# Kernel optimization log

Measured on AMD Instinct MI355X. Metric: run time of the kernel, lower is better.

## Reference

```python
import jax, jax.numpy as jnp
import numpy as np


def _rgcn(x, src, dst, et, basis, comp, root, bias):
    # Basis-decomposed RGCNConv (PyG semantics): per-relation mean aggregation
    # over incoming edges + root transform + bias.
    N = x.shape[0]
    R = comp.shape[0]
    W = jnp.einsum('rb,bio->rio', comp, basis)          # [R, in, out]
    xr = jnp.einsum('ni,rio->rno', x, W)                 # [R, N, out]
    msg = xr[et, src]                                    # [E, out] gather per edge
    seg = dst * R + et                                   # (target, relation) segment id
    cnt = jax.ops.segment_sum(jnp.ones(et.shape, x.dtype), seg, num_segments=N * R)
    norm = 1.0 / jnp.maximum(cnt, 1.0)                   # mean per (dst, relation)
    msg = msg * norm[seg][:, None]
    agg = jax.ops.segment_sum(msg, dst, num_segments=N)  # scatter-add to targets
    return agg + x @ root + bias


def setup_inputs() -> dict:
    key = jax.random.key(0)
    ks = jax.random.split(key, 20)
    N, E, R, B, F, D, C, NB = 100000, 1600000, 5, 512, 4, 32, 5, 2
    s = 0.1
    inp = {
        'x': jax.random.normal(ks[0], (N, F), jnp.float32),
        'edge_index': jax.random.randint(ks[1], (2, E), 0, N, dtype=jnp.int32),
        'edge_type': jax.random.randint(ks[2], (E,), 0, R, dtype=jnp.int32),
        'start_nodes': jax.random.randint(ks[3], (B,), 0, N, dtype=jnp.int32),
        # layer 0: in=F, out=D
        'basis0': jax.random.normal(ks[4], (NB, F, D), jnp.float32) * s,
        'comp0': jax.random.normal(ks[5], (R, NB), jnp.float32) * s,
        'root0': jax.random.normal(ks[6], (F, D), jnp.float32) * s,
        'bias0': jax.random.normal(ks[7], (D,), jnp.float32) * s,
        # layers 1..3: in=out=D, stacked
        'basis': jax.random.normal(ks[8], (3, NB, D, D), jnp.float32) * s,
        'comp': jax.random.normal(ks[9], (3, R, NB), jnp.float32) * s,
        'root': jax.random.normal(ks[10], (3, D, D), jnp.float32) * s,
        'bias': jax.random.normal(ks[11], (3, D), jnp.float32) * s,
        # MLP head: sum(latent_dim)=128 -> 128 -> C
        'lin1_w': jax.random.normal(ks[12], (4 * D, 128), jnp.float32) * s,
        'lin1_b': jax.random.normal(ks[13], (128,), jnp.float32) * s,
        'lin2_w': jax.random.normal(ks[14], (128, C), jnp.float32) * s,
        'lin2_b': jax.random.normal(ks[15], (C,), jnp.float32) * s,
    }
    return inp


def reference(x, edge_index, edge_type, start_nodes, basis0, comp0, root0, bias0,
              basis, comp, root, bias, lin1_w, lin1_b, lin2_w, lin2_b):
    src, dst = edge_index[0], edge_index[1]
    h = jnp.tanh(_rgcn(x, src, dst, edge_type, basis0, comp0, root0, bias0))
    states = [h]
    for l in range(basis.shape[0]):
        h = jnp.tanh(_rgcn(h, src, dst, edge_type, basis[l], comp[l], root[l], bias[l]))
        states.append(h)
    concat = jnp.concatenate(states, axis=1)             # [N, 128]
    # Per-graph readout: the walk's degenerate n_walks=1 branch, i.e. the
    # start (user) node's concatenated state (sequential backtracking walk
    # replaced by its deterministic initialization path; eval mode, no dropout).
    acc = concat[start_nodes]                            # [B, 128]
    h1 = jax.nn.relu(acc @ lin1_w + lin1_b)
    logits = h1 @ lin2_w + lin2_b
    return jax.nn.log_softmax(logits, axis=-1)
```

## Files before the change

kernel.cpp:

```cpp
#include <hip/hip_runtime.h>
#include <cstdint>

#define N_NODES 100000
#define N_EDGES 1600000
#define R_REL   5
#define NBASIS  2
#define B_START 512
#define PART_SZ 12500
#define NBUCK   256
#define BUCK_SZ 391
#define EPB     6250
#define STAGE_CAP 7000

typedef __attribute__((ext_vector_type(8))) short short8;
typedef __attribute__((ext_vector_type(4))) float f32x4;
typedef _Float16 half8 __attribute__((ext_vector_type(8)));

__device__ __forceinline__ unsigned short f2bf(float f) {
    unsigned u = __float_as_uint(f);
    unsigned r = (u + 0x7FFF + ((u >> 16) & 1)) >> 16;
    return (unsigned short)r;
}
__device__ __forceinline__ float bf2f(unsigned short u) {
    return __uint_as_float(((unsigned)u) << 16);
}
__device__ __forceinline__ unsigned short f2h(float f) {
    _Float16 h = (_Float16)f;
    return __builtin_bit_cast(unsigned short, h);
}


__global__ __launch_bounds__(256) void k_cntb(
    const int* __restrict__ ei, int* __restrict__ bhist) {
    __shared__ int lh[NBUCK];
    int tid = threadIdx.x;
    lh[tid] = 0;
    __syncthreads();
    int base = blockIdx.x * EPB;
    for (int j = tid; j < EPB; j += 256) {
        int dst = ei[N_EDGES + base + j];
        atomicAdd(&lh[dst / BUCK_SZ], 1);
    }
    __syncthreads();
    bhist[blockIdx.x * NBUCK + tid] = lh[tid];
}

__global__ __launch_bounds__(256) void k_colscan(
    int* __restrict__ bhist, int* __restrict__ colsum) {
    __shared__ int s[256];
    int b = blockIdx.x, i = threadIdx.x;
    int v = bhist[i * NBUCK + b];
    s[i] = v;
    __syncthreads();
    for (int o = 1; o < 256; o <<= 1) {
        int t = (i >= o) ? s[i - o] : 0;
        __syncthreads();
        s[i] += t;
        __syncthreads();
    }
    bhist[i * NBUCK + b] = s[i] - v;
    if (i == 255) colsum[b] = s[255];
}

__global__ __launch_bounds__(256) void k_tiny(
    const int* __restrict__ colsum, int* __restrict__ bbase) {
    __shared__ int s[256];
    int i = threadIdx.x;
    int v = colsum[i];
    s[i] = v;
    __syncthreads();
    for (int o = 1; o < 256; o <<= 1) {
        int t = (i >= o) ? s[i - o] : 0;
        __syncthreads();
        s[i] += t;
        __syncthreads();
    }
    bbase[i] = s[i] - v;
    if (i == 255) bbase[NBUCK] = s[255];
}

__global__ __launch_bounds__(256) void k_scat(
    const int* __restrict__ ei, const int* __restrict__ et,
    const int* __restrict__ bhist, const int* __restrict__ bbase,
    int* __restrict__ arena) {
    __shared__ int lc[NBUCK];
    int tid = threadIdx.x;
    lc[tid] = bhist[blockIdx.x * NBUCK + tid] + bbase[tid];
    __syncthreads();
    int base = blockIdx.x * EPB;
    for (int j = tid; j < EPB; j += 256) {
        int e   = base + j;
        int src = ei[e];
        int dst = ei[N_EDGES + e];
        int t   = et[e];
        int bk  = dst / BUCK_SZ;
        int dl  = dst - bk * BUCK_SZ;
        int pos = atomicAdd(&lc[bk], 1);
        arena[pos] = src | (t << 17) | (dl << 20);
    }
}

__global__ __launch_bounds__(256) void k_build(
    const int* __restrict__ arena, const int* __restrict__ bbase,
    int* __restrict__ off, int* __restrict__ pk_m, float* __restrict__ nv5,
    unsigned* __restrict__ degpk) {
    __shared__ int deg5[BUCK_SZ * R_REL];
    __shared__ int loff[BUCK_SZ + 1];
    __shared__ int cur5[BUCK_SZ * R_REL];
    __shared__ int stg[STAGE_CAP];
    __shared__ int tsum[256];
    int b = blockIdx.x, tid = threadIdx.x;
    int base = bbase[b], end = bbase[b + 1];
    int count = end - base;
    for (int i = tid; i < BUCK_SZ * R_REL; i += 256) deg5[i] = 0;
    __syncthreads();
    for (int i = tid; i < count; i += 256) {
        int r  = arena[base + i];
        int dl = ((unsigned)r) >> 20;
        int t  = (r >> 17) & 7;
        atomicAdd(&deg5[dl * R_REL + t], 1);
    }
    __syncthreads();
    for (int dl = tid; dl < BUCK_SZ; dl += 256) {
        loff[dl] = deg5[dl * R_REL + 0] + deg5[dl * R_REL + 1] +
                   deg5[dl * R_REL + 2] + deg5[dl * R_REL + 3] +
                   deg5[dl * R_REL + 4];
    }
    __syncthreads();
    int d0 = 2 * tid, d1 = 2 * tid + 1;
    int va = (d0 < BUCK_SZ) ? loff[d0] : 0;
    int vb = (d1 < BUCK_SZ) ? loff[d1] : 0;
    tsum[tid] = va + vb;
    __syncthreads();
    for (int o = 1; o < 256; o <<= 1) {
        int v = (tid >= o) ? tsum[tid - o] : 0;
        __syncthreads();
        tsum[tid] += v;
        __syncthreads();
    }
    int pre = tsum[tid] - (va + vb);
    if (d0 < BUCK_SZ) loff[d0] = pre;
    if (d1 < BUCK_SZ) loff[d1] = pre + va;
    __syncthreads();
    for (int dl = tid; dl < BUCK_SZ; dl += 256) {
        int nn = b * BUCK_SZ + dl;
        int run = loff[dl];
        unsigned dp = 0;
#pragma unroll
        for (int t = 0; t < R_REL; t++) {
            cur5[dl * R_REL + t] = run;
            int c = deg5[dl * R_REL + t];
            run += c;
            int cc = c > 63 ? 63 : c;
            dp |= ((unsigned)cc) << (6 * t);
        }
        if (nn < N_NODES) {
            off[nn]   = base + loff[dl];
            degpk[nn] = dp;
#pragma unroll
            for (int t = 0; t < R_REL; t++) {
                int c = deg5[dl * R_REL + t];
                nv5[nn * R_REL + t] = 1.0f / (float)(c > 0 ? c : 1);
            }
        }
    }
    if (b == NBUCK - 1 && tid == 0) off[N_NODES] = N_EDGES;
    __syncthreads();
    for (int i = tid; i < count; i += 256) {
        int r  = arena[base + i];
        int dl = ((unsigned)r) >> 20;
        int t  = (r >> 17) & 7;
        int rk = atomicAdd(&cur5[dl * R_REL + t], 1);
        if (rk < STAGE_CAP) stg[rk] = r;
    }
    __syncthreads();
    for (int i = tid; i < count; i += 256) {
        int r = stg[i < STAGE_CAP ? i : STAGE_CAP - 1];
        pk_m[base + i] = r & 0x1FFFF;
    }
}


__global__ __launch_bounds__(256) void k_wprep(
    const float* __restrict__ basis, const float* __restrict__ comp,
    const float* __restrict__ root,  const float* __restrict__ basis0,
    const float* __restrict__ comp0, const float* __restrict__ root0,
    unsigned short* __restrict__ wfh, unsigned short* __restrict__ wfr,
    unsigned short* __restrict__ wf0) {
    __shared__ float lw[5120];
    int tid = threadIdx.x;
    int l = blockIdx.x;
    if (l < 3) {
        for (int idx = tid; idx < 5120; idx += 256) {
            int r = idx >> 10, rem = idx & 1023, i = rem >> 5, o = rem & 31;
            lw[idx] = comp[l * 10 + r * 2 + 0] * basis[l * 2048 + i * 32 + o]
                    + comp[l * 10 + r * 2 + 1] * basis[l * 2048 + 1024 + i * 32 + o];
        }
        __syncthreads();
        for (int idx = tid; idx < 5120; idx += 256) {
            int ot = idx / 2560, rem = idx % 2560;
            int s = rem >> 9, ln = (rem >> 3) & 63, j = idx & 7;
            int o = ot * 16 + (ln & 15), kk = (ln >> 4) * 8 + j;
            wfh[l * 5120 + idx] = f2h(lw[s * 1024 + kk * 32 + o]);
        }
        for (int idx = tid; idx < 2048; idx += 256) {
            int ot = idx >> 10, s = (idx >> 9) & 1, ln = (idx >> 3) & 63, j = idx & 7;
            int o = ot * 16 + (ln & 15), kk = (ln >> 4) * 8 + j;
            float val = root[l * 1024 + kk * 32 + o];
            unsigned short hi = f2bf(val);
            wfr[l * 2048 + idx] = s ? f2bf(val - bf2f(hi)) : hi;
        }
    } else {
        for (int idx = tid; idx < 1024; idx += 256) {
            int k = idx >> 5, o = idx & 31;
            float val = 0.f;
            if (k < 20) {
                int r = k >> 2, i = k & 3;
                val = comp0[r * 2 + 0] * basis0[i * 32 + o]
                    + comp0[r * 2 + 1] * basis0[128 + i * 32 + o];
            } else if (k < 24) val = root0[(k - 20) * 32 + o];
            lw[idx] = val;
        }
        __syncthreads();
        for (int idx = tid; idx < 1024; idx += 256) {
            int ot = idx >> 9, ln = (idx >> 3) & 63, j = idx & 7;
            int o = ot * 16 + (ln & 15), kk = (ln >> 4) * 8 + j;
            wf0[idx] = f2h(lw[kk * 32 + o]);
        }
    }
}


__global__ __launch_bounds__(256) void k_cvt0(
    const float* __restrict__ x, unsigned short* __restrict__ hb0) {
    int n = blockIdx.x * 256 + threadIdx.x;
    if (n >= N_NODES) return;
    float4 xv = *(const float4*)(x + (size_t)n * 4);
    unsigned short h0 = f2bf(xv.x), h1 = f2bf(xv.y), h2 = f2bf(xv.z), h3 = f2bf(xv.w);
    unsigned long long ph = (unsigned long long)h0 | ((unsigned long long)h1 << 16)
                          | ((unsigned long long)h2 << 32) | ((unsigned long long)h3 << 48);
    *(unsigned long long*)(hb0 + (size_t)n * 4) = ph;
}


__global__ __launch_bounds__(256) void k_gath32(
    const unsigned short* __restrict__ hb, const int* __restrict__ pk_m,
    const float* __restrict__ nv5, const unsigned* __restrict__ degpk,
    const int* __restrict__ off, unsigned short* __restrict__ agg) {
    int tid  = threadIdx.x;
    int lane32 = tid & 31;
    int sub  = tid >> 5;
    int part  = blockIdx.x & 7;
    int local = (blockIdx.x >> 3) * 8 + sub;
    if (local >= PART_SZ) return;
    int n = part * PART_SZ + local;
    int cpos = lane32 & 7;
    int slot = lane32 >> 3;
    const uint2* __restrict__ hb2 = (const uint2*)hb;

    int e0 = off[n];
    unsigned dp = degpk[n];
    int chunkbase = e0;
    int mreg = (chunkbase + lane32 < N_EDGES) ? pk_m[chunkbase + lane32] : 0;
    int e = e0;
#pragma unroll
    for (int r = 0; r < R_REL; r++) {
        int cnt = (int)((dp >> (6 * r)) & 63u);
        float nv = nv5[n * R_REL + r];
        float a0 = 0.f, a1 = 0.f, a2 = 0.f, a3 = 0.f;
        for (int kb = 0; kb < cnt; kb += 4) {
            if (e + kb + 3 >= chunkbase + 32) {
                chunkbase = e + kb;
                mreg = (chunkbase + lane32 < N_EDGES) ? pk_m[chunkbase + lane32] : 0;
            }
            int kq = kb + slot;
            int mq = __shfl(mreg, e + kq - chunkbase, 32);
            uint2 u = hb2[(size_t)mq * 8 + cpos];
            float msk = (kq < cnt) ? nv : 0.f;
            a0 += msk * __uint_as_float(u.x << 16);
            a1 += msk * __uint_as_float(u.x & 0xFFFF0000u);
            a2 += msk * __uint_as_float(u.y << 16);
            a3 += msk * __uint_as_float(u.y & 0xFFFF0000u);
        }
        e += cnt;
        a0 += __shfl_xor(a0, 8, 32);  a0 += __shfl_xor(a0, 16, 32);
        a1 += __shfl_xor(a1, 8, 32);  a1 += __shfl_xor(a1, 16, 32);
        a2 += __shfl_xor(a2, 8, 32);  a2 += __shfl_xor(a2, 16, 32);
        a3 += __shfl_xor(a3, 8, 32);  a3 += __shfl_xor(a3, 16, 32);
        if (slot == 0) {
            uint2 pk;
            pk.x = (unsigned)f2h(a0) | ((unsigned)f2h(a1) << 16);
            pk.y = (unsigned)f2h(a2) | ((unsigned)f2h(a3) << 16);
            *(uint2*)(agg + (size_t)n * 160 + r * 32 + cpos * 4) = pk;
        }
    }
}


__global__ __launch_bounds__(256) void k_gath0(
    const unsigned short* __restrict__ hb0, const float* __restrict__ x,
    const int* __restrict__ pk_m, const float* __restrict__ nv5,
    const unsigned* __restrict__ degpk, const int* __restrict__ off,
    unsigned short* __restrict__ a0v) {
    int tid  = threadIdx.x;
    int lane32 = tid & 31;
    int sub  = tid >> 5;
    int part  = blockIdx.x & 7;
    int local = (blockIdx.x >> 3) * 8 + sub;
    if (local >= PART_SZ) return;
    int n = part * PART_SZ + local;
    int cpos = lane32 & 1;
    int slot = lane32 >> 1;
    const unsigned* __restrict__ hb32 = (const unsigned*)hb0;

    int e0 = off[n];
    unsigned dp = degpk[n];
    int chunkbase = e0;
    int mreg = (chunkbase + lane32 < N_EDGES) ? pk_m[chunkbase + lane32] : 0;
    int e = e0;
#pragma unroll
    for (int r = 0; r < R_REL; r++) {
        int cnt = (int)((dp >> (6 * r)) & 63u);
        float nv = nv5[n * R_REL + r];
        float p0 = 0.f, p1 = 0.f;
        for (int kb = 0; kb < cnt; kb += 16) {
            if (e + kb + 15 >= chunkbase + 32) {
                chunkbase = e + kb;
                mreg = (chunkbase + lane32 < N_EDGES) ? pk_m[chunkbase + lane32] : 0;
            }
            int kq = kb + slot;
            int mq = __shfl(mreg, e + kq - chunkbase, 32);
            unsigned u = hb32[(size_t)mq * 2 + cpos];
            float msk = (kq < cnt) ? nv : 0.f;
            p0 += msk * __uint_as_float(u << 16);
            p1 += msk * __uint_as_float(u & 0xFFFF0000u);
        }
        e += cnt;
        p0 += __shfl_xor(p0, 2, 32); p0 += __shfl_xor(p0, 4, 32);
        p0 += __shfl_xor(p0, 8, 32); p0 += __shfl_xor(p0, 16, 32);
        p1 += __shfl_xor(p1, 2, 32); p1 += __shfl_xor(p1, 4, 32);
        p1 += __shfl_xor(p1, 8, 32); p1 += __shfl_xor(p1, 16, 32);
        if (slot == 0) {
            unsigned pk = (unsigned)f2h(p0) | ((unsigned)f2h(p1) << 16);
            *(unsigned*)(a0v + (size_t)n * 32 + r * 4 + cpos * 2) = pk;
        }
    }
    if (lane32 < 12) {
        float xv = (lane32 < 4) ? x[(size_t)n * 4 + lane32] : 0.f;
        a0v[(size_t)n * 32 + 20 + lane32] = (lane32 < 4) ? f2h(xv) : (unsigned short)0;
    }
}


__global__ __launch_bounds__(256) void k_gemm(
    const unsigned short* __restrict__ agg, const unsigned short* __restrict__ hbin,
    const unsigned short* __restrict__ wfhl, const unsigned short* __restrict__ wfrl,
    const float* __restrict__ biasL, float* __restrict__ h,
    unsigned short* __restrict__ hbout) {
    int tid = threadIdx.x;
    int wid = tid >> 6, lane = tid & 63;
    int tile = blockIdx.x * 4 + wid;
    if (tile >= N_NODES / 16) return;
    int n0 = tile * 16;
    int row = lane & 15, kg = lane >> 4;
    const half8* ar = (const half8*)(agg + (size_t)(n0 + row) * 160 + kg * 8);
    const half8* wh = (const half8*)wfhl;
    const short8* wr = (const short8*)wfrl;
    short8 hbf = *(const short8*)(hbin + (size_t)(n0 + row) * 32 + kg * 8);
    f32x4 c0 = {0.f, 0.f, 0.f, 0.f}, c1 = {0.f, 0.f, 0.f, 0.f};
#pragma unroll
    for (int s = 0; s < 5; s++) {
        half8 a = ar[s * 4];
        c0 = __builtin_amdgcn_mfma_f32_16x16x32_f16(a, wh[s * 64 + lane], c0, 0, 0, 0);
        c1 = __builtin_amdgcn_mfma_f32_16x16x32_f16(a, wh[320 + s * 64 + lane], c1, 0, 0, 0);
    }
    c0 = __builtin_amdgcn_mfma_f32_16x16x32_bf16(hbf, wr[lane], c0, 0, 0, 0);
    c0 = __builtin_amdgcn_mfma_f32_16x16x32_bf16(hbf, wr[64 + lane], c0, 0, 0, 0);
    c1 = __builtin_amdgcn_mfma_f32_16x16x32_bf16(hbf, wr[128 + lane], c1, 0, 0, 0);
    c1 = __builtin_amdgcn_mfma_f32_16x16x32_bf16(hbf, wr[192 + lane], c1, 0, 0, 0);
    float b0 = biasL[row], b1 = biasL[16 + row];
#pragma unroll
    for (int i = 0; i < 4; i++) {
        int n = n0 + kg * 4 + i;
        float t0 = tanhf(c0[i] + b0);
        float t1 = tanhf(c1[i] + b1);
        h[(size_t)n * 32 + row]      = t0;
        h[(size_t)n * 32 + 16 + row] = t1;
        hbout[(size_t)n * 32 + row]      = f2bf(t0);
        hbout[(size_t)n * 32 + 16 + row] = f2bf(t1);
    }
}

__global__ __launch_bounds__(256) void k_gemm0(
    const unsigned short* __restrict__ a0v, const unsigned short* __restrict__ wf0,
    const float* __restrict__ biasL, float* __restrict__ h,
    unsigned short* __restrict__ hbout) {
    int tid = threadIdx.x;
    int wid = tid >> 6, lane = tid & 63;
    int tile = blockIdx.x * 4 + wid;
    if (tile >= N_NODES / 16) return;
    int n0 = tile * 16;
    int row = lane & 15, kg = lane >> 4;
    half8 a = *(const half8*)(a0v + (size_t)(n0 + row) * 32 + kg * 8);
    const half8* wv = (const half8*)wf0;
    f32x4 c0 = {0.f, 0.f, 0.f, 0.f}, c1 = {0.f, 0.f, 0.f, 0.f};
    c0 = __builtin_amdgcn_mfma_f32_16x16x32_f16(a, wv[lane], c0, 0, 0, 0);
    c1 = __builtin_amdgcn_mfma_f32_16x16x32_f16(a, wv[64 + lane], c1, 0, 0, 0);
    float b0 = biasL[row], b1 = biasL[16 + row];
#pragma unroll
    for (int i = 0; i < 4; i++) {
        int n = n0 + kg * 4 + i;
        float t0 = tanhf(c0[i] + b0);
        float t1 = tanhf(c1[i] + b1);
        h[(size_t)n * 32 + row]      = t0;
        h[(size_t)n * 32 + 16 + row] = t1;
        hbout[(size_t)n * 32 + row]      = f2bf(t0);
        hbout[(size_t)n * 32 + 16 + row] = f2bf(t1);
    }
}


__global__ void k_save(const float* __restrict__ h, const int* __restrict__ start,
                       float* __restrict__ sav) {
    int t = blockIdx.x * blockDim.x + threadIdx.x;
    if (t < B_START * 32) {
        int b = t >> 5, ln = t & 31;
        sav[t] = h[(size_t)start[b] * 32 + ln];
    }
}

__global__ __launch_bounds__(128) void k_mlp(
    const float* __restrict__ sav, const float* __restrict__ w1,
    const float* __restrict__ b1, const float* __restrict__ w2,
    const float* __restrict__ b2, float* __restrict__ out) {
    __shared__ float cvec[128];
    __shared__ float hb[128];
    __shared__ float lg[8];
    int b = blockIdx.x, t = threadIdx.x;
    cvec[t] = sav[(t >> 5) * (B_START * 32) + b * 32 + (t & 31)];
    __syncthreads();
    float a = b1[t];
#pragma unroll 8
    for (int k = 0; k < 128; k++) a += cvec[k] * w1[k * 128 + t];
    hb[t] = fmaxf(a, 0.f);
    __syncthreads();
    if (t < 5) {
        float a2 = b2[t];
        for (int k = 0; k < 128; k++) a2 += hb[k] * w2[k * 5 + t];
        lg[t] = a2;
    }
    __syncthreads();
    if (t < 5) {
        float m = lg[0];
        for (int j = 1; j < 5; j++) m = fmaxf(m, lg[j]);
        float s = 0.f;
        for (int j = 0; j < 5; j++) s += expf(lg[j] - m);
        out[b * 5 + t] = lg[t] - m - logf(s);
    }
}


extern "C" void kernel_launch(void* const* d_in, const int* in_sizes, int n_in,
                              void* d_out, int out_size, void* d_ws, size_t ws_size,
                              hipStream_t stream) {
    const float* x      = (const float*)d_in[0];
    const int*   ei     = (const int*)d_in[1];
    const int*   etype  = (const int*)d_in[2];
    const int*   start  = (const int*)d_in[3];
    const float* basis0 = (const float*)d_in[4];
    const float* comp0  = (const float*)d_in[5];
    const float* root0  = (const float*)d_in[6];
    const float* bias0  = (const float*)d_in[7];
    const float* basis  = (const float*)d_in[8];
    const float* comp   = (const float*)d_in[9];
    const float* root   = (const float*)d_in[10];
    const float* bias   = (const float*)d_in[11];
    const float* w1     = (const float*)d_in[12];
    const float* b1     = (const float*)d_in[13];
    const float* w2     = (const float*)d_in[14];
    const float* b2     = (const float*)d_in[15];
    float* out = (float*)d_out;

    char* p = (char*)d_ws;
    auto alloc = [&](size_t bytes) -> void* {
        void* r = (void*)p;
        p += (bytes + 255) & ~(size_t)255;
        return r;
    };
    int*            bhist  = (int*)alloc((size_t)NBUCK * NBUCK * 4);
    int*            colsum = (int*)alloc(NBUCK * 4);
    int*            bbase  = (int*)alloc((NBUCK + 1) * 4);
    int*            arena  = (int*)alloc((size_t)N_EDGES * 4);
    int*            off    = (int*)alloc((N_NODES + 1) * 4);
    int*            pk_m   = (int*)alloc((size_t)N_EDGES * 4);
    float*          nv5    = (float*)alloc((size_t)N_NODES * R_REL * 4);
    unsigned*       degpk  = (unsigned*)alloc((size_t)N_NODES * 4);
    float*          h      = (float*)alloc((size_t)N_NODES * 32 * 4);
    unsigned short* hbuf   = (unsigned short*)alloc((size_t)(N_NODES + 64) * 32 * 2);
    unsigned short* hb0    = (unsigned short*)alloc((size_t)N_NODES * 4 * 2);
    unsigned short* a0v    = (unsigned short*)alloc((size_t)(N_NODES + 64) * 32 * 2);
    unsigned short* agg    = (unsigned short*)alloc((size_t)(N_NODES + 64) * 160 * 2);
    unsigned short* wfh    = (unsigned short*)alloc((size_t)3 * 5120 * 2);
    unsigned short* wfr    = (unsigned short*)alloc((size_t)3 * 2048 * 2);
    unsigned short* wf0    = (unsigned short*)alloc((size_t)1024 * 2);
    float*          sav    = (float*)alloc(4 * B_START * 32 * 4);

    k_cntb<<<NBUCK, 256, 0, stream>>>(ei, bhist);
    k_colscan<<<NBUCK, 256, 0, stream>>>(bhist, colsum);
    k_tiny<<<1, 256, 0, stream>>>(colsum, bbase);
    k_scat<<<NBUCK, 256, 0, stream>>>(ei, etype, bhist, bbase, arena);
    k_build<<<NBUCK, 256, 0, stream>>>(arena, bbase, off, pk_m, nv5, degpk);
    k_wprep<<<4, 256, 0, stream>>>(basis, comp, root, basis0, comp0, root0,
                                   wfh, wfr, wf0);
    k_cvt0<<<(N_NODES + 255) / 256, 256, 0, stream>>>(x, hb0);

    int nbGath = 8 * ((PART_SZ + 7) / 8);
    int nbGemm = (N_NODES / 16 + 3) / 4;

    k_gath0<<<nbGath, 256, 0, stream>>>(hb0, x, pk_m, nv5, degpk, off, a0v);
    k_gemm0<<<nbGemm, 256, 0, stream>>>(a0v, wf0, bias0, h, hbuf);
    k_save<<<64, 256, 0, stream>>>(h, start, sav);
    for (int l = 0; l < 3; l++) {
        k_gath32<<<nbGath, 256, 0, stream>>>(hbuf, pk_m, nv5, degpk, off, agg);
        k_gemm<<<nbGemm, 256, 0, stream>>>(agg, hbuf, wfh + (size_t)l * 5120,
                                           wfr + (size_t)l * 2048, bias + l * 32,
                                           h, hbuf);
        k_save<<<64, 256, 0, stream>>>(h, start, sav + (l + 1) * 16384);
    }

    k_mlp<<<B_START, 128, 0, stream>>>(sav, w1, b1, w2, b2, out);
}
```

Before: 380.1 us.

## Assign one lane group per relation in gather kernels with prefetched indices

The gather kernels are restructured so that each relation of a node gets its own group of lanes. Each group walks that relation's edges sequentially, prefetching the next edge index, and uses wider 16-byte or 8-byte feature loads. This replaces the old scheme of shuffle-broadcast edge chunks, masked slots and cross-slot shuffle reductions, which wasted lanes on low-degree relations. It also drops the partition-interleaved block mapping and adds nontemporal loads and stores for the streamed index and aggregate buffers. In exchange, per-lane serial loops follow per-relation degree, which may cause divergence and imbalance, and the three lanes with s >= 5 in each 8-lane group sit idle.

```diff
diff --git a/kernel.cpp b/kernel.cpp
--- a/kernel.cpp
+++ b/kernel.cpp
@@ -6,7 +6,6 @@
 #define R_REL   5
 #define NBASIS  2
 #define B_START 512
-#define PART_SZ 12500
 #define NBUCK   256
 #define BUCK_SZ 391
 #define EPB     6250
@@ -15,6 +14,8 @@
 typedef __attribute__((ext_vector_type(8))) short short8;
 typedef __attribute__((ext_vector_type(4))) float f32x4;
 typedef _Float16 half8 __attribute__((ext_vector_type(8)));
+typedef unsigned uint32x2 __attribute__((ext_vector_type(2)));
+typedef unsigned uint32x4 __attribute__((ext_vector_type(4)));
 
 __device__ __forceinline__ unsigned short f2bf(float f) {
     unsigned u = __float_as_uint(f);
@@ -247,52 +248,50 @@
     const unsigned short* __restrict__ hb, const int* __restrict__ pk_m,
     const float* __restrict__ nv5, const unsigned* __restrict__ degpk,
     const int* __restrict__ off, unsigned short* __restrict__ agg) {
-    int tid  = threadIdx.x;
+    int tid = threadIdx.x;
+    int n = blockIdx.x * 8 + (tid >> 5);
     int lane32 = tid & 31;
-    int sub  = tid >> 5;
-    int part  = blockIdx.x & 7;
-    int local = (blockIdx.x >> 3) * 8 + sub;
-    if (local >= PART_SZ) return;
-    int n = part * PART_SZ + local;
-    int cpos = lane32 & 7;
-    int slot = lane32 >> 3;
-    const uint2* __restrict__ hb2 = (const uint2*)hb;
+    int s = lane32 >> 2;
+    int cpos = lane32 & 3;
 
     int e0 = off[n];
     unsigned dp = degpk[n];
-    int chunkbase = e0;
-    int mreg = (chunkbase + lane32 < N_EDGES) ? pk_m[chunkbase + lane32] : 0;
-    int e = e0;
-#pragma unroll
-    for (int r = 0; r < R_REL; r++) {
-        int cnt = (int)((dp >> (6 * r)) & 63u);
-        float nv = nv5[n * R_REL + r];
-        float a0 = 0.f, a1 = 0.f, a2 = 0.f, a3 = 0.f;
-        for (int kb = 0; kb < cnt; kb += 4) {
-            if (e + kb + 3 >= chunkbase + 32) {
-                chunkbase = e + kb;
-                mreg = (chunkbase + lane32 < N_EDGES) ? pk_m[chunkbase + lane32] : 0;
-            }
-            int kq = kb + slot;
-            int mq = __shfl(mreg, e + kq - chunkbase, 32);
-            uint2 u = hb2[(size_t)mq * 8 + cpos];
-            float msk = (kq < cnt) ? nv : 0.f;
-            a0 += msk * __uint_as_float(u.x << 16);
-            a1 += msk * __uint_as_float(u.x & 0xFFFF0000u);
-            a2 += msk * __uint_as_float(u.y << 16);
-            a3 += msk * __uint_as_float(u.y & 0xFFFF0000u);
-        }
-        e += cnt;
-        a0 += __shfl_xor(a0, 8, 32);  a0 += __shfl_xor(a0, 16, 32);
-        a1 += __shfl_xor(a1, 8, 32);  a1 += __shfl_xor(a1, 16, 32);
-        a2 += __shfl_xor(a2, 8, 32);  a2 += __shfl_xor(a2, 16, 32);
-        a3 += __shfl_xor(a3, 8, 32);  a3 += __shfl_xor(a3, 16, 32);
-        if (slot == 0) {
-            uint2 pk;
-            pk.x = (unsigned)f2h(a0) | ((unsigned)f2h(a1) << 16);
-            pk.y = (unsigned)f2h(a2) | ((unsigned)f2h(a3) << 16);
-            *(uint2*)(agg + (size_t)n * 160 + r * 32 + cpos * 4) = pk;
-        }
+    int c0 = dp & 63, c1 = (dp >> 6) & 63, c2 = (dp >> 12) & 63,
+        c3 = (dp >> 18) & 63, c4 = (dp >> 24) & 63;
+    int cnt = s == 0 ? c0 : s == 1 ? c1 : s == 2 ? c2 : s == 3 ? c3
+            : s == 4 ? c4 : 0;
+    int start = (s > 0 ? c0 : 0) + (s > 1 ? c1 : 0) + (s > 2 ? c2 : 0)
+              + (s > 3 ? c3 : 0);
+    float nv = (s < R_REL) ? nv5[n * R_REL + s] : 0.f;
+
+    const uint32x4* __restrict__ hb4 = (const uint32x4*)hb;
+    float a0 = 0.f, a1 = 0.f, a2 = 0.f, a3 = 0.f;
+    float a4 = 0.f, a5 = 0.f, a6 = 0.f, a7 = 0.f;
+    int base = e0 + start;
+    int pb = base < N_EDGES ? base : N_EDGES - 1;
+    int mcur = __builtin_nontemporal_load(pk_m + pb);
+    for (int k = 0; k < cnt; ++k) {
+        int kn = k + 1 < cnt ? k + 1 : cnt - 1;
+        int mnxt = __builtin_nontemporal_load(pk_m + base + kn);
+        uint32x4 u = hb4[(size_t)mcur * 4 + cpos];
+        a0 += nv * __uint_as_float(u.x << 16);
+        a1 += nv * __uint_as_float(u.x & 0xFFFF0000u);
+        a2 += nv * __uint_as_float(u.y << 16);
+        a3 += nv * __uint_as_float(u.y & 0xFFFF0000u);
+        a4 += nv * __uint_as_float(u.z << 16);
+        a5 += nv * __uint_as_float(u.z & 0xFFFF0000u);
+        a6 += nv * __uint_as_float(u.w << 16);
+        a7 += nv * __uint_as_float(u.w & 0xFFFF0000u);
+        mcur = mnxt;
+    }
+    if (s < R_REL) {
+        uint32x4 pk;
+        pk.x = (unsigned)f2h(a0) | ((unsigned)f2h(a1) << 16);
+        pk.y = (unsigned)f2h(a2) | ((unsigned)f2h(a3) << 16);
+        pk.z = (unsigned)f2h(a4) | ((unsigned)f2h(a5) << 16);
+        pk.w = (unsigned)f2h(a6) | ((unsigned)f2h(a7) << 16);
+        __builtin_nontemporal_store(pk,
+            (uint32x4*)(agg + (size_t)n * 160 + s * 32 + cpos * 8));
     }
 }
 
@@ -302,52 +301,53 @@
     const int* __restrict__ pk_m, const float* __restrict__ nv5,
     const unsigned* __restrict__ degpk, const int* __restrict__ off,
     unsigned short* __restrict__ a0v) {
-    int tid  = threadIdx.x;
-    int lane32 = tid & 31;
-    int sub  = tid >> 5;
-    int part  = blockIdx.x & 7;
-    int local = (blockIdx.x >> 3) * 8 + sub;
-    if (local >= PART_SZ) return;
-    int n = part * PART_SZ + local;
-    int cpos = lane32 & 1;
-    int slot = lane32 >> 1;
-    const unsigned* __restrict__ hb32 = (const unsigned*)hb0;
+    int tid = threadIdx.x;
+    int n = blockIdx.x * 32 + (tid >> 3);
+    int s = tid & 7;
 
     int e0 = off[n];
     unsigned dp = degpk[n];
-    int chunkbase = e0;
-    int mreg = (chunkbase + lane32 < N_EDGES) ? pk_m[chunkbase + lane32] : 0;
-    int e = e0;
-#pragma unroll
-    for (int r = 0; r < R_REL; r++) {
-        int cnt = (int)((dp >> (6 * r)) & 63u);
-        float nv = nv5[n * R_REL + r];
-        float p0 = 0.f, p1 = 0.f;
-        for (int kb = 0; kb < cnt; kb += 16) {
-            if (e + kb + 15 >= chunkbase + 32) {
-                chunkbase = e + kb;
-                mreg = (chunkbase + lane32 < N_EDGES) ? pk_m[chunkbase + lane32] : 0;
-            }
-            int kq = kb + slot;
-            int mq = __shfl(mreg, e + kq - chunkbase, 32);
-            unsigned u = hb32[(size_t)mq * 2 + cpos];
-            float msk = (kq < cnt) ? nv : 0.f;
-            p0 += msk * __uint_as_float(u << 16);
-            p1 += msk * __uint_as_float(u & 0xFFFF0000u);
-        }
-        e += cnt;
-        p0 += __shfl_xor(p0, 2, 32); p0 += __shfl_xor(p0, 4, 32);
-        p0 += __shfl_xor(p0, 8, 32); p0 += __shfl_xor(p0, 16, 32);
-        p1 += __shfl_xor(p1, 2, 32); p1 += __shfl_xor(p1, 4, 32);
-        p1 += __shfl_xor(p1, 8, 32); p1 += __shfl_xor(p1, 16, 32);
-        if (slot == 0) {
-            unsigned pk = (unsigned)f2h(p0) | ((unsigned)f2h(p1) << 16);
-            *(unsigned*)(a0v + (size_t)n * 32 + r * 4 + cpos * 2) = pk;
-        }
-    }
-    if (lane32 < 12) {
-        float xv = (lane32 < 4) ? x[(size_t)n * 4 + lane32] : 0.f;
-        a0v[(size_t)n * 32 + 20 + lane32] = (lane32 < 4) ? f2h(xv) : (unsigned short)0;
+    int c0 = dp & 63, c1 = (dp >> 6) & 63, c2 = (dp >> 12) & 63,
+        c3 = (dp >> 18) & 63, c4 = (dp >> 24) & 63;
+    int cnt = s == 0 ? c0 : s == 1 ? c1 : s == 2 ? c2 : s == 3 ? c3
+            : s == 4 ? c4 : 0;
+    int start = (s > 0 ? c0 : 0) + (s > 1 ? c1 : 0) + (s > 2 ? c2 : 0)
+              + (s > 3 ? c3 : 0);
+    float nv = (s < R_REL) ? nv5[n * R_REL + s] : 0.f;
+
+    const uint32x2* __restrict__ hb2 = (const uint32x2*)hb0;
+    float a0 = 0.f, a1 = 0.f, a2 = 0.f, a3 = 0.f;
+    int base = e0 + start;
+    int pb = base < N_EDGES ? base : N_EDGES - 1;
+    int mcur = __builtin_nontemporal_load(pk_m + pb);
+    for (int k = 0; k < cnt; ++k) {
+        int kn = k + 1 < cnt ? k + 1 : cnt - 1;
+        int mnxt = __builtin_nontemporal_load(pk_m + base + kn);
+        uint32x2 u = hb2[mcur];
+        a0 += nv * __uint_as_float(u.x << 16);
+        a1 += nv * __uint_as_float(u.x & 0xFFFF0000u);
+        a2 += nv * __uint_as_float(u.y << 16);
+        a3 += nv * __uint_as_float(u.y & 0xFFFF0000u);
+        mcur = mnxt;
+    }
+    if (s < R_REL) {
+        uint32x2 pk;
+        pk.x = (unsigned)f2h(a0) | ((unsigned)f2h(a1) << 16);
+        pk.y = (unsigned)f2h(a2) | ((unsigned)f2h(a3) << 16);
+        __builtin_nontemporal_store(pk,
+            (uint32x2*)(a0v + (size_t)n * 32 + s * 4));
+    } else if (s == 5) {
+        float4 xv = *(const float4*)(x + (size_t)n * 4);
+        uint32x2 pk;
+        pk.x = (unsigned)f2h(xv.x) | ((unsigned)f2h(xv.y) << 16);
+        pk.y = (unsigned)f2h(xv.z) | ((unsigned)f2h(xv.w) << 16);
+        __builtin_nontemporal_store(pk,
+            (uint32x2*)(a0v + (size_t)n * 32 + 20));
+    } else {
+        uint32x2 z;
+        z.x = 0u; z.y = 0u;
+        __builtin_nontemporal_store(z,
+            (uint32x2*)(a0v + (size_t)n * 32 + 24 + (s - 6) * 4));
     }
 }
 
@@ -370,7 +370,7 @@
     f32x4 c0 = {0.f, 0.f, 0.f, 0.f}, c1 = {0.f, 0.f, 0.f, 0.f};
 #pragma unroll
     for (int s = 0; s < 5; s++) {
-        half8 a = ar[s * 4];
+        half8 a = __builtin_nontemporal_load(&ar[s * 4]);
         c0 = __builtin_amdgcn_mfma_f32_16x16x32_f16(a, wh[s * 64 + lane], c0, 0, 0, 0);
         c1 = __builtin_amdgcn_mfma_f32_16x16x32_f16(a, wh[320 + s * 64 + lane], c1, 0, 0, 0);
     }
@@ -514,14 +514,13 @@
                                    wfh, wfr, wf0);
     k_cvt0<<<(N_NODES + 255) / 256, 256, 0, stream>>>(x, hb0);
 
-    int nbGath = 8 * ((PART_SZ + 7) / 8);
     int nbGemm = (N_NODES / 16 + 3) / 4;
 
-    k_gath0<<<nbGath, 256, 0, stream>>>(hb0, x, pk_m, nv5, degpk, off, a0v);
+    k_gath0<<<N_NODES / 32, 256, 0, stream>>>(hb0, x, pk_m, nv5, degpk, off, a0v);
     k_gemm0<<<nbGemm, 256, 0, stream>>>(a0v, wf0, bias0, h, hbuf);
     k_save<<<64, 256, 0, stream>>>(h, start, sav);
     for (int l = 0; l < 3; l++) {
-        k_gath32<<<nbGath, 256, 0, stream>>>(hbuf, pk_m, nv5, degpk, off, agg);
+        k_gath32<<<N_NODES / 8, 256, 0, stream>>>(hbuf, pk_m, nv5, degpk, off, agg);
         k_gemm<<<nbGemm, 256, 0, stream>>>(agg, hbuf, wfh + (size_t)l * 5120,
                                            wfr + (size_t)l * 2048, bias + l * 32,
                                            h, hbuf);
```

New measurement: 407.0 us. 1.07x slower.

## Split hidden-state features into two halves and gather each in separate passes

Applied to the files above, without the earlier changes.

The bf16 hidden-state buffer is split into two 16-feature arrays, and the 32-wide gather kernel is replaced by two 16-wide gather launches, one per half. Each half-array is half the size, so random gathers within one pass should hit L2/MALL more often. The cost is reading the edge index list twice and launching twice as many gather kernels. Index loads and the agg stores/loads also become nontemporal hints.

```diff
diff --git a/kernel.cpp b/kernel.cpp
--- a/kernel.cpp
+++ b/kernel.cpp
@@ -15,6 +15,8 @@
 typedef __attribute__((ext_vector_type(8))) short short8;
 typedef __attribute__((ext_vector_type(4))) float f32x4;
 typedef _Float16 half8 __attribute__((ext_vector_type(8)));
+typedef unsigned uint32x2 __attribute__((ext_vector_type(2)));
+typedef unsigned uint32x4 __attribute__((ext_vector_type(4)));
 
 __device__ __forceinline__ unsigned short f2bf(float f) {
     unsigned u = __float_as_uint(f);
@@ -243,8 +245,9 @@
 }
 
 
-__global__ __launch_bounds__(256) void k_gath32(
-    const unsigned short* __restrict__ hb, const int* __restrict__ pk_m,
+template <int HALF>
+__global__ __launch_bounds__(256) void k_gath16(
+    const unsigned short* __restrict__ hbh, const int* __restrict__ pk_m,
     const float* __restrict__ nv5, const unsigned* __restrict__ degpk,
     const int* __restrict__ off, unsigned short* __restrict__ agg) {
     int tid  = threadIdx.x;
@@ -254,28 +257,30 @@
     int local = (blockIdx.x >> 3) * 8 + sub;
     if (local >= PART_SZ) return;
     int n = part * PART_SZ + local;
-    int cpos = lane32 & 7;
-    int slot = lane32 >> 3;
-    const uint2* __restrict__ hb2 = (const uint2*)hb;
+    int cpos = lane32 & 3;
+    int slot = lane32 >> 2;
+    const uint32x2* __restrict__ hb2 = (const uint32x2*)hbh;
 
     int e0 = off[n];
     unsigned dp = degpk[n];
     int chunkbase = e0;
-    int mreg = (chunkbase + lane32 < N_EDGES) ? pk_m[chunkbase + lane32] : 0;
+    int mreg = (chunkbase + lane32 < N_EDGES)
+             ? __builtin_nontemporal_load(pk_m + chunkbase + lane32) : 0;
     int e = e0;
 #pragma unroll
     for (int r = 0; r < R_REL; r++) {
         int cnt = (int)((dp >> (6 * r)) & 63u);
         float nv = nv5[n * R_REL + r];
         float a0 = 0.f, a1 = 0.f, a2 = 0.f, a3 = 0.f;
-        for (int kb = 0; kb < cnt; kb += 4) {
-            if (e + kb + 3 >= chunkbase + 32) {
+        for (int kb = 0; kb < cnt; kb += 8) {
+            if (e + kb + 7 >= chunkbase + 32) {
                 chunkbase = e + kb;
-                mreg = (chunkbase + lane32 < N_EDGES) ? pk_m[chunkbase + lane32] : 0;
+                mreg = (chunkbase + lane32 < N_EDGES)
+                     ? __builtin_nontemporal_load(pk_m + chunkbase + lane32) : 0;
             }
             int kq = kb + slot;
             int mq = __shfl(mreg, e + kq - chunkbase, 32);
-            uint2 u = hb2[(size_t)mq * 8 + cpos];
+            uint32x2 u = hb2[(size_t)mq * 4 + cpos];
             float msk = (kq < cnt) ? nv : 0.f;
             a0 += msk * __uint_as_float(u.x << 16);
             a1 += msk * __uint_as_float(u.x & 0xFFFF0000u);
@@ -283,15 +288,16 @@
             a3 += msk * __uint_as_float(u.y & 0xFFFF0000u);
         }
         e += cnt;
-        a0 += __shfl_xor(a0, 8, 32);  a0 += __shfl_xor(a0, 16, 32);
-        a1 += __shfl_xor(a1, 8, 32);  a1 += __shfl_xor(a1, 16, 32);
-        a2 += __shfl_xor(a2, 8, 32);  a2 += __shfl_xor(a2, 16, 32);
-        a3 += __shfl_xor(a3, 8, 32);  a3 += __shfl_xor(a3, 16, 32);
+        a0 += __shfl_xor(a0, 4, 32); a0 += __shfl_xor(a0, 8, 32); a0 += __shfl_xor(a0, 16, 32);
+        a1 += __shfl_xor(a1, 4, 32); a1 += __shfl_xor(a1, 8, 32); a1 += __shfl_xor(a1, 16, 32);
+        a2 += __shfl_xor(a2, 4, 32); a2 += __shfl_xor(a2, 8, 32); a2 += __shfl_xor(a2, 16, 32);
+        a3 += __shfl_xor(a3, 4, 32); a3 += __shfl_xor(a3, 8, 32); a3 += __shfl_xor(a3, 16, 32);
         if (slot == 0) {
-            uint2 pk;
+            uint32x2 pk;
             pk.x = (unsigned)f2h(a0) | ((unsigned)f2h(a1) << 16);
             pk.y = (unsigned)f2h(a2) | ((unsigned)f2h(a3) << 16);
-            *(uint2*)(agg + (size_t)n * 160 + r * 32 + cpos * 4) = pk;
+            __builtin_nontemporal_store(pk,
+                (uint32x2*)(agg + (size_t)n * 160 + r * 32 + HALF * 16 + cpos * 4));
         }
     }
 }
@@ -316,7 +322,8 @@
     int e0 = off[n];
     unsigned dp = degpk[n];
     int chunkbase = e0;
-    int mreg = (chunkbase + lane32 < N_EDGES) ? pk_m[chunkbase + lane32] : 0;
+    int mreg = (chunkbase + lane32 < N_EDGES)
+             ? __builtin_nontemporal_load(pk_m + chunkbase + lane32) : 0;
     int e = e0;
 #pragma unroll
     for (int r = 0; r < R_REL; r++) {
@@ -326,7 +333,8 @@
         for (int kb = 0; kb < cnt; kb += 16) {
             if (e + kb + 15 >= chunkbase + 32) {
                 chunkbase = e + kb;
-                mreg = (chunkbase + lane32 < N_EDGES) ? pk_m[chunkbase + lane32] : 0;
+                mreg = (chunkbase + lane32 < N_EDGES)
+                     ? __builtin_nontemporal_load(pk_m + chunkbase + lane32) : 0;
             }
             int kq = kb + slot;
             int mq = __shfl(mreg, e + kq - chunkbase, 32);
@@ -353,10 +361,11 @@
 
 
 __global__ __launch_bounds__(256) void k_gemm(
-    const unsigned short* __restrict__ agg, const unsigned short* __restrict__ hbin,
-    const unsigned short* __restrict__ wfhl, const unsigned short* __restrict__ wfrl,
-    const float* __restrict__ biasL, float* __restrict__ h,
-    unsigned short* __restrict__ hbout) {
+    const unsigned short* __restrict__ agg, const unsigned short* __restrict__ hbL,
+    const unsigned short* __restrict__ hbH, const unsigned short* __restrict__ wfhl,
+    const unsigned short* __restrict__ wfrl, const float* __restrict__ biasL,
+    float* __restrict__ h, unsigned short* __restrict__ hbLo,
+    unsigned short* __restrict__ hbHo) {
     int tid = threadIdx.x;
     int wid = tid >> 6, lane = tid & 63;
     int tile = blockIdx.x * 4 + wid;
@@ -366,11 +375,14 @@
     const half8* ar = (const half8*)(agg + (size_t)(n0 + row) * 160 + kg * 8);
     const half8* wh = (const half8*)wfhl;
     const short8* wr = (const short8*)wfrl;
-    short8 hbf = *(const short8*)(hbin + (size_t)(n0 + row) * 32 + kg * 8);
+    const unsigned short* hsrc = (kg < 2)
+        ? hbL + (size_t)(n0 + row) * 16 + kg * 8
+        : hbH + (size_t)(n0 + row) * 16 + (kg - 2) * 8;
+    short8 hbf = *(const short8*)hsrc;
     f32x4 c0 = {0.f, 0.f, 0.f, 0.f}, c1 = {0.f, 0.f, 0.f, 0.f};
 #pragma unroll
     for (int s = 0; s < 5; s++) {
-        half8 a = ar[s * 4];
+        half8 a = __builtin_nontemporal_load(&ar[s * 4]);
         c0 = __builtin_amdgcn_mfma_f32_16x16x32_f16(a, wh[s * 64 + lane], c0, 0, 0, 0);
         c1 = __builtin_amdgcn_mfma_f32_16x16x32_f16(a, wh[320 + s * 64 + lane], c1, 0, 0, 0);
     }
@@ -386,15 +398,15 @@
         float t1 = tanhf(c1[i] + b1);
         h[(size_t)n * 32 + row]      = t0;
         h[(size_t)n * 32 + 16 + row] = t1;
-        hbout[(size_t)n * 32 + row]      = f2bf(t0);
-        hbout[(size_t)n * 32 + 16 + row] = f2bf(t1);
+        hbLo[(size_t)n * 16 + row] = f2bf(t0);
+        hbHo[(size_t)n * 16 + row] = f2bf(t1);
     }
 }
 
 __global__ __launch_bounds__(256) void k_gemm0(
     const unsigned short* __restrict__ a0v, const unsigned short* __restrict__ wf0,
     const float* __restrict__ biasL, float* __restrict__ h,
-    unsigned short* __restrict__ hbout) {
+    unsigned short* __restrict__ hbLo, unsigned short* __restrict__ hbHo) {
     int tid = threadIdx.x;
     int wid = tid >> 6, lane = tid & 63;
     int tile = blockIdx.x * 4 + wid;
@@ -414,8 +426,8 @@
         float t1 = tanhf(c1[i] + b1);
         h[(size_t)n * 32 + row]      = t0;
         h[(size_t)n * 32 + 16 + row] = t1;
-        hbout[(size_t)n * 32 + row]      = f2bf(t0);
-        hbout[(size_t)n * 32 + 16 + row] = f2bf(t1);
+        hbLo[(size_t)n * 16 + row] = f2bf(t0);
+        hbHo[(size_t)n * 16 + row] = f2bf(t1);
     }
 }
 
@@ -496,7 +508,8 @@
     float*          nv5    = (float*)alloc((size_t)N_NODES * R_REL * 4);
     unsigned*       degpk  = (unsigned*)alloc((size_t)N_NODES * 4);
     float*          h      = (float*)alloc((size_t)N_NODES * 32 * 4);
-    unsigned short* hbuf   = (unsigned short*)alloc((size_t)(N_NODES + 64) * 32 * 2);
+    unsigned short* hbL    = (unsigned short*)alloc((size_t)(N_NODES + 64) * 16 * 2);
+    unsigned short* hbH    = (unsigned short*)alloc((size_t)(N_NODES + 64) * 16 * 2);
     unsigned short* hb0    = (unsigned short*)alloc((size_t)N_NODES * 4 * 2);
     unsigned short* a0v    = (unsigned short*)alloc((size_t)(N_NODES + 64) * 32 * 2);
     unsigned short* agg    = (unsigned short*)alloc((size_t)(N_NODES + 64) * 160 * 2);
@@ -518,13 +531,14 @@
     int nbGemm = (N_NODES / 16 + 3) / 4;
 
     k_gath0<<<nbGath, 256, 0, stream>>>(hb0, x, pk_m, nv5, degpk, off, a0v);
-    k_gemm0<<<nbGemm, 256, 0, stream>>>(a0v, wf0, bias0, h, hbuf);
+    k_gemm0<<<nbGemm, 256, 0, stream>>>(a0v, wf0, bias0, h, hbL, hbH);
     k_save<<<64, 256, 0, stream>>>(h, start, sav);
     for (int l = 0; l < 3; l++) {
-        k_gath32<<<nbGath, 256, 0, stream>>>(hbuf, pk_m, nv5, degpk, off, agg);
-        k_gemm<<<nbGemm, 256, 0, stream>>>(agg, hbuf, wfh + (size_t)l * 5120,
+        k_gath16<0><<<nbGath, 256, 0, stream>>>(hbL, pk_m, nv5, degpk, off, agg);
+        k_gath16<1><<<nbGath, 256, 0, stream>>>(hbH, pk_m, nv5, degpk, off, agg);
+        k_gemm<<<nbGemm, 256, 0, stream>>>(agg, hbL, hbH, wfh + (size_t)l * 5120,
                                            wfr + (size_t)l * 2048, bias + l * 32,
-                                           h, hbuf);
+                                           h, hbL, hbH);
         k_save<<<64, 256, 0, stream>>>(h, start, sav + (l + 1) * 16384);
     }
 
```

New measurement: 529.3 us. 39.3% more time.

## Restructure 32-wide gather to 8 lanes per node with unrolled edge loop

Applied to the files above, without the earlier changes.

The hidden-layer gather kernel now assigns 8 lanes per node (one per 4-feature chunk) instead of a 32-lane group with 4 edge slots. Each thread walks all incoming edges itself, with the first 32 fully unrolled, so many row loads are in flight at once. Relation membership is resolved through per-edge masks into five accumulator sets, which removes the cross-lane shuffle reductions and chunked index reloads. Index loads and agg stores use nontemporal hints, also in gath0 and the GEMM. The cost is more registers and redundant index loads across the 8 lanes, and the block indexing drops the old partition interleave.

```diff
diff --git a/kernel.cpp b/kernel.cpp
--- a/kernel.cpp
+++ b/kernel.cpp
@@ -11,10 +11,12 @@
 #define BUCK_SZ 391
 #define EPB     6250
 #define STAGE_CAP 7000
+#define UNR     32
 
 typedef __attribute__((ext_vector_type(8))) short short8;
 typedef __attribute__((ext_vector_type(4))) float f32x4;
 typedef _Float16 half8 __attribute__((ext_vector_type(8)));
+typedef unsigned uint32x2 __attribute__((ext_vector_type(2)));
 
 __device__ __forceinline__ unsigned short f2bf(float f) {
     unsigned u = __float_as_uint(f);
@@ -247,52 +249,80 @@
     const unsigned short* __restrict__ hb, const int* __restrict__ pk_m,
     const float* __restrict__ nv5, const unsigned* __restrict__ degpk,
     const int* __restrict__ off, unsigned short* __restrict__ agg) {
-    int tid  = threadIdx.x;
-    int lane32 = tid & 31;
-    int sub  = tid >> 5;
-    int part  = blockIdx.x & 7;
-    int local = (blockIdx.x >> 3) * 8 + sub;
-    if (local >= PART_SZ) return;
-    int n = part * PART_SZ + local;
-    int cpos = lane32 & 7;
-    int slot = lane32 >> 3;
-    const uint2* __restrict__ hb2 = (const uint2*)hb;
+    int tid = threadIdx.x;
+    int n = blockIdx.x * 32 + (tid >> 3);
+    int cpos = tid & 7;
+    const uint32x2* __restrict__ hb2 = (const uint32x2*)hb;
 
     int e0 = off[n];
     unsigned dp = degpk[n];
-    int chunkbase = e0;
-    int mreg = (chunkbase + lane32 < N_EDGES) ? pk_m[chunkbase + lane32] : 0;
-    int e = e0;
+    int b1 = dp & 63;
+    int b2 = b1 + ((dp >> 6) & 63);
+    int b3 = b2 + ((dp >> 12) & 63);
+    int b4 = b3 + ((dp >> 18) & 63);
+    int deg = b4 + ((dp >> 24) & 63);
+    float nv0 = nv5[n * R_REL + 0];
+    float nv1 = nv5[n * R_REL + 1];
+    float nv2 = nv5[n * R_REL + 2];
+    float nv3 = nv5[n * R_REL + 3];
+    float nv4 = nv5[n * R_REL + 4];
+
+    int m[UNR];
+#pragma unroll
+    for (int k = 0; k < UNR; k++) {
+        m[k] = 0;
+        if (k < deg) m[k] = __builtin_nontemporal_load(pk_m + e0 + k);
+    }
+
+    float ax[R_REL], ay[R_REL], az[R_REL], aw[R_REL];
+#pragma unroll
+    for (int r = 0; r < R_REL; r++) { ax[r] = 0.f; ay[r] = 0.f; az[r] = 0.f; aw[r] = 0.f; }
+
+#pragma unroll
+    for (int k = 0; k < UNR; k++) {
+        if (k < deg) {
+            uint32x2 u = hb2[(size_t)m[k] * 8 + cpos];
+            float vx = __uint_as_float(u.x << 16);
+            float vy = __uint_as_float(u.x & 0xFFFF0000u);
+            float vz = __uint_as_float(u.y << 16);
+            float vw = __uint_as_float(u.y & 0xFFFF0000u);
+            float w0 = (k < b1) ? nv0 : 0.f;
+            float w1 = (k >= b1 && k < b2) ? nv1 : 0.f;
+            float w2 = (k >= b2 && k < b3) ? nv2 : 0.f;
+            float w3 = (k >= b3 && k < b4) ? nv3 : 0.f;
+            float w4 = (k >= b4) ? nv4 : 0.f;
+            ax[0] += w0 * vx; ay[0] += w0 * vy; az[0] += w0 * vz; aw[0] += w0 * vw;
+            ax[1] += w1 * vx; ay[1] += w1 * vy; az[1] += w1 * vz; aw[1] += w1 * vw;
+            ax[2] += w2 * vx; ay[2] += w2 * vy; az[2] += w2 * vz; aw[2] += w2 * vw;
+            ax[3] += w3 * vx; ay[3] += w3 * vy; az[3] += w3 * vz; aw[3] += w3 * vw;
+            ax[4] += w4 * vx; ay[4] += w4 * vy; az[4] += w4 * vz; aw[4] += w4 * vw;
+        }
+    }
+    for (int k = UNR; k < deg; k++) {
+        int mk = __builtin_nontemporal_load(pk_m + e0 + k);
+        uint32x2 u = hb2[(size_t)mk * 8 + cpos];
+        float vx = __uint_as_float(u.x << 16);
+        float vy = __uint_as_float(u.x & 0xFFFF0000u);
+        float vz = __uint_as_float(u.y << 16);
+        float vw = __uint_as_float(u.y & 0xFFFF0000u);
+        float w0 = (k < b1) ? nv0 : 0.f;
+        float w1 = (k >= b1 && k < b2) ? nv1 : 0.f;
+        float w2 = (k >= b2 && k < b3) ? nv2 : 0.f;
+        float w3 = (k >= b3 && k < b4) ? nv3 : 0.f;
+        float w4 = (k >= b4) ? nv4 : 0.f;
+        ax[0] += w0 * vx; ay[0] += w0 * vy; az[0] += w0 * vz; aw[0] += w0 * vw;
+        ax[1] += w1 * vx; ay[1] += w1 * vy; az[1] += w1 * vz; aw[1] += w1 * vw;
+        ax[2] += w2 * vx; ay[2] += w2 * vy; az[2] += w2 * vz; aw[2] += w2 * vw;
+        ax[3] += w3 * vx; ay[3] += w3 * vy; az[3] += w3 * vz; aw[3] += w3 * vw;
+        ax[4] += w4 * vx; ay[4] += w4 * vy; az[4] += w4 * vz; aw[4] += w4 * vw;
+    }
 #pragma unroll
     for (int r = 0; r < R_REL; r++) {
-        int cnt = (int)((dp >> (6 * r)) & 63u);
-        float nv = nv5[n * R_REL + r];
-        float a0 = 0.f, a1 = 0.f, a2 = 0.f, a3 = 0.f;
-        for (int kb = 0; kb < cnt; kb += 4) {
-            if (e + kb + 3 >= chunkbase + 32) {
-                chunkbase = e + kb;
-                mreg = (chunkbase + lane32 < N_EDGES) ? pk_m[chunkbase + lane32] : 0;
-            }
-            int kq = kb + slot;
-            int mq = __shfl(mreg, e + kq - chunkbase, 32);
-            uint2 u = hb2[(size_t)mq * 8 + cpos];
-            float msk = (kq < cnt) ? nv : 0.f;
-            a0 += msk * __uint_as_float(u.x << 16);
-            a1 += msk * __uint_as_float(u.x & 0xFFFF0000u);
-            a2 += msk * __uint_as_float(u.y << 16);
-            a3 += msk * __uint_as_float(u.y & 0xFFFF0000u);
-        }
-        e += cnt;
-        a0 += __shfl_xor(a0, 8, 32);  a0 += __shfl_xor(a0, 16, 32);
-        a1 += __shfl_xor(a1, 8, 32);  a1 += __shfl_xor(a1, 16, 32);
-        a2 += __shfl_xor(a2, 8, 32);  a2 += __shfl_xor(a2, 16, 32);
-        a3 += __shfl_xor(a3, 8, 32);  a3 += __shfl_xor(a3, 16, 32);
-        if (slot == 0) {
-            uint2 pk;
-            pk.x = (unsigned)f2h(a0) | ((unsigned)f2h(a1) << 16);
-            pk.y = (unsigned)f2h(a2) | ((unsigned)f2h(a3) << 16);
-            *(uint2*)(agg + (size_t)n * 160 + r * 32 + cpos * 4) = pk;
-        }
+        uint32x2 pk;
+        pk.x = (unsigned)f2h(ax[r]) | ((unsigned)f2h(ay[r]) << 16);
+        pk.y = (unsigned)f2h(az[r]) | ((unsigned)f2h(aw[r]) << 16);
+        __builtin_nontemporal_store(pk,
+            (uint32x2*)(agg + (size_t)n * 160 + r * 32 + cpos * 4));
     }
 }
 
@@ -316,7 +346,8 @@
     int e0 = off[n];
     unsigned dp = degpk[n];
     int chunkbase = e0;
-    int mreg = (chunkbase + lane32 < N_EDGES) ? pk_m[chunkbase + lane32] : 0;
+    int mreg = (chunkbase + lane32 < N_EDGES)
+             ? __builtin_nontemporal_load(pk_m + chunkbase + lane32) : 0;
     int e = e0;
 #pragma unroll
     for (int r = 0; r < R_REL; r++) {
@@ -326,7 +357,8 @@
         for (int kb = 0; kb < cnt; kb += 16) {
             if (e + kb + 15 >= chunkbase + 32) {
                 chunkbase = e + kb;
-                mreg = (chunkbase + lane32 < N_EDGES) ? pk_m[chunkbase + lane32] : 0;
+                mreg = (chunkbase + lane32 < N_EDGES)
+                     ? __builtin_nontemporal_load(pk_m + chunkbase + lane32) : 0;
             }
             int kq = kb + slot;
             int mq = __shfl(mreg, e + kq - chunkbase, 32);
@@ -370,7 +402,7 @@
     f32x4 c0 = {0.f, 0.f, 0.f, 0.f}, c1 = {0.f, 0.f, 0.f, 0.f};
 #pragma unroll
     for (int s = 0; s < 5; s++) {
-        half8 a = ar[s * 4];
+        half8 a = __builtin_nontemporal_load(&ar[s * 4]);
         c0 = __builtin_amdgcn_mfma_f32_16x16x32_f16(a, wh[s * 64 + lane], c0, 0, 0, 0);
         c1 = __builtin_amdgcn_mfma_f32_16x16x32_f16(a, wh[320 + s * 64 + lane], c1, 0, 0, 0);
     }
@@ -521,7 +553,7 @@
     k_gemm0<<<nbGemm, 256, 0, stream>>>(a0v, wf0, bias0, h, hbuf);
     k_save<<<64, 256, 0, stream>>>(h, start, sav);
     for (int l = 0; l < 3; l++) {
-        k_gath32<<<nbGath, 256, 0, stream>>>(hbuf, pk_m, nv5, degpk, off, agg);
+        k_gath32<<<N_NODES / 32, 256, 0, stream>>>(hbuf, pk_m, nv5, degpk, off, agg);
         k_gemm<<<nbGemm, 256, 0, stream>>>(agg, hbuf, wfh + (size_t)l * 5120,
                                            wfr + (size_t)l * 2048, bias + l * 32,
                                            h, hbuf);
```

After: 410.3 us. 7.9% more time.
